# Kernel tuning notes

Hardware: AMD Instinct MI355X
Metric: run time of the kernel (lower is better)

Reference implementation:

```python
import jax, jax.numpy as jnp
import numpy as np

H = 16
D_MODEL = 1024
D_K = D_MODEL // H  # 64


def setup_inputs() -> dict:
    key = jax.random.key(0)
    ks = jax.random.split(key, 8)
    B, S = 8, 1024
    q = jax.random.normal(ks[0], (B, S, D_MODEL), dtype=jnp.float32)
    k = jax.random.normal(ks[1], (B, S, D_MODEL), dtype=jnp.float32)
    v = jax.random.normal(ks[2], (B, S, D_MODEL), dtype=jnp.float32)
    # xavier_normal for [h, d_model, d_k]: std = sqrt(2 / (d_model + d_k)) (fan over last two dims)
    std_p = float(np.sqrt(2.0 / (D_MODEL + D_K)))
    W_q = jax.random.normal(ks[3], (H, D_MODEL, D_K), dtype=jnp.float32) * std_p
    W_k = jax.random.normal(ks[4], (H, D_MODEL, D_K), dtype=jnp.float32) * std_p
    W_v = jax.random.normal(ks[5], (H, D_MODEL, D_K), dtype=jnp.float32) * std_p
    std_o = float(np.sqrt(2.0 / (H * D_K + D_MODEL)))
    W_o = jax.random.normal(ks[6], (D_MODEL, H * D_K), dtype=jnp.float32) * std_o  # torch Linear weight [out, in]
    b_o = jax.random.normal(ks[7], (D_MODEL,), dtype=jnp.float32) * 0.01
    return {"q": q, "k": k, "v": v, "W_q": W_q, "W_k": W_k, "W_v": W_v, "W_o": W_o, "b_o": b_o}


def reference(q, k, v, W_q, W_k, W_v, W_o, b_o):
    B, S, _ = q.shape
    # per-head projections: [h, b, s, d_k]
    qh = jnp.einsum('bsd,hdk->hbsk', q, W_q)
    kh = jnp.einsum('bsd,hdk->hbsk', k, W_k)
    vh = jnp.einsum('bsd,hdk->hbsk', v, W_v)
    scale = 1.0 / jnp.sqrt(jnp.asarray(D_K, dtype=q.dtype))
    scores = jnp.einsum('hbsk,hbtk->hbst', qh, kh) * scale  # [h,b,s,s]
    attn = jax.nn.softmax(scores, axis=-1)
    c = jnp.einsum('hbst,hbtk->hbsk', attn, vh)  # [h,b,s,d_k]
    # torch code splits the stacked (h*b) batch and concats on feature dim:
    # head index becomes the OUTER factor of the feature dim -> [b,s,h*d_k]
    c = jnp.transpose(c, (1, 2, 0, 3)).reshape(B, S, H * D_K)
    out = c @ W_o.T + b_o
    return out
```

## Files before the change

### kernel.cpp

```cpp
#include <hip/hip_runtime.h>
#include <hip/hip_bf16.h>

typedef __bf16 bf16_t;
typedef __attribute__((ext_vector_type(8))) __bf16 bf16x8;
typedef __attribute__((ext_vector_type(4))) float f32x4;

#define MFMA(a, b, c) __builtin_amdgcn_mfma_f32_16x16x32_bf16(a, b, c, 0, 0, 0)

__device__ inline void gload_lds16(const bf16_t* g, bf16_t* l) {
  __builtin_amdgcn_global_load_lds(
      (const __attribute__((address_space(1))) void*)g,
      (__attribute__((address_space(3))) void*)l, 16, 0, 0);
}

__global__ void fill_sentinel(float* out, int n, float val) {
  int i = blockIdx.x * blockDim.x + threadIdx.x;
  if (i < n) out[i] = val;
}

__global__ void transpose_w(const float* __restrict__ Wq, const float* __restrict__ Wk,
                            const float* __restrict__ Wv, bf16_t* __restrict__ Wt) {
  int gid = blockIdx.x * blockDim.x + threadIdx.x;
  int e = gid * 8;
  int m = e >> 20;
  int rem = e & 1048575;
  int n = rem >> 10;
  int d0 = rem & 1023;
  const float* W = (m == 0) ? Wq : (m == 1) ? Wk : Wv;
  int h = n >> 6, kk = n & 63;
  union { bf16_t h8[8]; uint4 u; } tmp;
#pragma unroll
  for (int j = 0; j < 8; ++j)
    tmp.h8[j] = (bf16_t)W[((size_t)(h * 1024 + d0 + j)) * 64 + kk];
  *(uint4*)(Wt + e) = tmp.u;
}

__global__ void cvt_bf16(const float* __restrict__ in, bf16_t* __restrict__ out) {
  size_t i = (size_t)(blockIdx.x * blockDim.x + threadIdx.x) * 8;
  f32x4 a = *(const f32x4*)(in + i);
  f32x4 b = *(const f32x4*)(in + i + 4);
  bf16x8 r;
  r[0] = (bf16_t)a[0]; r[1] = (bf16_t)a[1]; r[2] = (bf16_t)a[2]; r[3] = (bf16_t)a[3];
  r[4] = (bf16_t)b[0]; r[5] = (bf16_t)b[1]; r[6] = (bf16_t)b[2]; r[7] = (bf16_t)b[3];
  *(bf16x8*)(out + i) = r;
}

template <int MODE>
__global__ void gemm_bt(const bf16_t* __restrict__ A, const bf16_t* __restrict__ Bt_,
                        const float* __restrict__ bias, void* __restrict__ out_) {
  __shared__ bf16_t sA[2][64 * 32];
  __shared__ bf16_t sB[2][128 * 32];
  const int t = threadIdx.x;
  const int w = t >> 6, l = t & 63;
  const int lq = l >> 4, ll = l & 15;
  const int m0 = blockIdx.x * 64, n0 = blockIdx.y * 128;
  const bf16_t* Bt = (MODE == 0 && m0 >= 8192) ? Bt_ + 1048576 : Bt_;
  const float scale = (MODE == 0 && m0 < 8192) ? 0.125f : 1.0f;
  const int srow = l >> 2;
  const int scol = (l & 3) * 8;
  f32x4 acc[4][2] = {};

  auto stage = [&](int bufi, int k0s) {
    gload_lds16(A + (size_t)(m0 + w * 16 + srow) * 1024 + k0s + scol,
                sA[bufi] + w * 512);
#pragma unroll
    for (int c = 0; c < 2; ++c) {
      int ch = w * 2 + c;
      gload_lds16(Bt + (size_t)(n0 + ch * 16 + srow) * 1024 + k0s + scol,
                  sB[bufi] + ch * 512);
    }
  };

  stage(0, 0);
  __syncthreads();

  int cur = 0;
  for (int k0 = 0; k0 < 1024; k0 += 32) {
    if (k0 + 32 < 1024) stage(cur ^ 1, k0 + 32);
    bf16x8 af[4], bfr[2];
#pragma unroll
    for (int i = 0; i < 4; ++i)
      af[i] = *(const bf16x8*)(sA[cur] + (i * 16 + ll) * 32 + lq * 8);
#pragma unroll
    for (int i = 0; i < 2; ++i)
      bfr[i] = *(const bf16x8*)(sB[cur] + (w * 32 + i * 16 + ll) * 32 + lq * 8);
#pragma unroll
    for (int mi = 0; mi < 4; ++mi)
#pragma unroll
      for (int ni = 0; ni < 2; ++ni)
        acc[mi][ni] = MFMA(af[mi], bfr[ni], acc[mi][ni]);
    __syncthreads();
    cur ^= 1;
  }
#pragma unroll
  for (int mi = 0; mi < 4; ++mi)
#pragma unroll
    for (int ni = 0; ni < 2; ++ni)
#pragma unroll
      for (int r = 0; r < 4; ++r) {
        int row = m0 + mi * 16 + lq * 4 + r;
        int col = n0 + w * 32 + ni * 16 + ll;
        float v = acc[mi][ni][r];
        if (MODE == 2) {
          ((float*)out_)[(size_t)row * 1024 + col] = v + bias[col];
        } else if (MODE == 1) {
          int h = col >> 6, kk = col & 63, b = row >> 10, s = row & 1023;
          ((bf16_t*)out_)[((size_t)((h * 8 + b) * 64 + kk)) * 1024 + s] = (bf16_t)v;
        } else {
          int mat = row >> 13, rr = row & 8191;
          int h = col >> 6, kk = col & 63, b = rr >> 10, s = rr & 1023;
          size_t idx = (size_t)mat * 8388608 +
                       ((size_t)((h * 8 + b) * 1024 + s)) * 64 + kk;
          ((bf16_t*)out_)[idx] = (bf16_t)(v * scale);
        }
      }
}

__global__ void attn_kernel(const bf16_t* __restrict__ qh, const bf16_t* __restrict__ kh,
                            const bf16_t* __restrict__ vt, bf16_t* __restrict__ c) {
  constexpr int KP = 72, PP = 72;
  __shared__ bf16_t sK[2][64 * KP];
  __shared__ bf16_t sP[4][16 * PP];
  const int t = threadIdx.x;
  const int w = t >> 6, l = t & 63;
  const int lq = l >> 4, ll = l & 15;
  const int orig = blockIdx.x + (blockIdx.y << 4);
  const int wg = (orig & 7) * 256 + (orig >> 3);
  const int q0 = (wg & 15) * 64;
  const int hb = wg >> 4;
  const int h = hb >> 3, b = hb & 7;
  const size_t base = (size_t)hb * 65536;
  const bf16_t* Q = qh + base + (size_t)q0 * 64;
  const bf16_t* K = kh + base;
  const bf16_t* V = vt + base;

  bf16x8 aq0 = *(const bf16x8*)(Q + (w * 16 + ll) * 64 + 0 * 32 + lq * 8);
  bf16x8 aq1 = *(const bf16x8*)(Q + (w * 16 + ll) * 64 + 1 * 32 + lq * 8);

  {
    int e0 = t * 8, e1 = (256 + t) * 8;
    uint4 ka = *(const uint4*)(K + e0);
    uint4 kb = *(const uint4*)(K + e1);
    *(uint4*)(sK[0] + (e0 >> 6) * KP + (e0 & 63)) = ka;
    *(uint4*)(sK[0] + (e1 >> 6) * KP + (e1 & 63)) = kb;
  }
  __syncthreads();

  float mrow = -1e30f, lrow = 0.f;
  f32x4 o[4] = {};
  bf16_t* Pw = sP[w];

  int cur = 0;
  for (int kt = 0; kt < 1024; kt += 64, cur ^= 1) {
    uint4 kr0, kr1;
    if (kt < 960) {
      kr0 = *(const uint4*)(K + (size_t)(kt + 64) * 64 + t * 8);
      kr1 = *(const uint4*)(K + (size_t)(kt + 64) * 64 + (256 + t) * 8);
    }
    const bf16_t* Vb = V + (size_t)ll * 1024 + kt + lq * 8;
    bf16x8 bv00 = *(const bf16x8*)(Vb + 0 * 16384 + 0);
    bf16x8 bv01 = *(const bf16x8*)(Vb + 1 * 16384 + 0);
    bf16x8 bv02 = *(const bf16x8*)(Vb + 2 * 16384 + 0);
    bf16x8 bv03 = *(const bf16x8*)(Vb + 3 * 16384 + 0);
    bf16x8 bv10 = *(const bf16x8*)(Vb + 0 * 16384 + 32);
    bf16x8 bv11 = *(const bf16x8*)(Vb + 1 * 16384 + 32);
    bf16x8 bv12 = *(const bf16x8*)(Vb + 2 * 16384 + 32);
    bf16x8 bv13 = *(const bf16x8*)(Vb + 3 * 16384 + 32);

    f32x4 sacc[4] = {};
    __builtin_amdgcn_s_setprio(1);
#pragma unroll
    for (int ni = 0; ni < 4; ++ni) {
      bf16x8 bk0 = *(const bf16x8*)(sK[cur] + (ni * 16 + ll) * KP + 0 * 32 + lq * 8);
      bf16x8 bk1 = *(const bf16x8*)(sK[cur] + (ni * 16 + ll) * KP + 1 * 32 + lq * 8);
      sacc[ni] = MFMA(bk0, aq0, sacc[ni]);
      sacc[ni] = MFMA(bk1, aq1, sacc[ni]);
    }
    __builtin_amdgcn_s_setprio(0);
    float rmax = -1e30f;
#pragma unroll
    for (int ni = 0; ni < 4; ++ni)
#pragma unroll
      for (int r = 0; r < 4; ++r)
        rmax = fmaxf(rmax, sacc[ni][r]);
    if (!__all(rmax <= mrow + 8.0f)) {
      rmax = fmaxf(rmax, __shfl_xor(rmax, 16));
      rmax = fmaxf(rmax, __shfl_xor(rmax, 32));
      float mnew = fmaxf(mrow, rmax);
      float alpha = __expf(mrow - mnew);
      mrow = mnew;
      lrow *= alpha;
#pragma unroll
      for (int r = 0; r < 4; ++r) {
        float ar = __shfl(alpha, lq * 4 + r, 16);
#pragma unroll
        for (int ni = 0; ni < 4; ++ni)
          o[ni][r] *= ar;
      }
    }
#pragma unroll
    for (int ni = 0; ni < 4; ++ni)
#pragma unroll
      for (int r = 0; r < 4; ++r) {
        float p = __expf(sacc[ni][r] - mrow);
        sacc[ni][r] = p;
        lrow += p;
      }
#pragma unroll
    for (int ni = 0; ni < 4; ++ni) {
      union { bf16_t h4[4]; uint2 u; } pk;
      pk.h4[0] = (bf16_t)sacc[ni][0];
      pk.h4[1] = (bf16_t)sacc[ni][1];
      pk.h4[2] = (bf16_t)sacc[ni][2];
      pk.h4[3] = (bf16_t)sacc[ni][3];
      *(uint2*)(Pw + ll * PP + ni * 16 + lq * 4) = pk.u;
    }
    asm volatile("s_waitcnt lgkmcnt(0)" ::: "memory");
    __builtin_amdgcn_sched_barrier(0);
    bf16x8 ap0 = *(const bf16x8*)(Pw + ll * PP + 0 * 32 + lq * 8);
    bf16x8 ap1 = *(const bf16x8*)(Pw + ll * PP + 1 * 32 + lq * 8);
    __builtin_amdgcn_s_setprio(1);
    o[0] = MFMA(ap0, bv00, o[0]);
    o[1] = MFMA(ap0, bv01, o[1]);
    o[2] = MFMA(ap0, bv02, o[2]);
    o[3] = MFMA(ap0, bv03, o[3]);
    o[0] = MFMA(ap1, bv10, o[0]);
    o[1] = MFMA(ap1, bv11, o[1]);
    o[2] = MFMA(ap1, bv12, o[2]);
    o[3] = MFMA(ap1, bv13, o[3]);
    __builtin_amdgcn_s_setprio(0);
    if (kt < 960) {
      int e0 = t * 8, e1 = (256 + t) * 8;
      *(uint4*)(sK[cur ^ 1] + (e0 >> 6) * KP + (e0 & 63)) = kr0;
      *(uint4*)(sK[cur ^ 1] + (e1 >> 6) * KP + (e1 & 63)) = kr1;
    }
    __syncthreads();
  }
  lrow += __shfl_xor(lrow, 16);
  lrow += __shfl_xor(lrow, 32);
#pragma unroll
  for (int r = 0; r < 4; ++r) {
    float lr = __shfl(lrow, lq * 4 + r, 16);
    int s = q0 + w * 16 + lq * 4 + r;
#pragma unroll
    for (int ni = 0; ni < 4; ++ni) {
      int dk = ni * 16 + ll;
      c[((size_t)(b * 1024 + s)) * 1024 + h * 64 + dk] = (bf16_t)(o[ni][r] / lr);
    }
  }
}

extern "C" void kernel_launch(void* const* d_in, const int* in_sizes, int n_in,
                              void* d_out, int out_size, void* d_ws, size_t ws_size,
                              hipStream_t stream) {
  float* out = (float*)d_out;
  int nblk_out = (out_size + 255) / 256;
  if (n_in != 8) {
    fill_sentinel<<<nblk_out, 256, 0, stream>>>(out, out_size, 600.0f + 10.0f * n_in);
    return;
  }
  const int expect[8] = {8388608, 8388608, 8388608, 1048576,
                         1048576, 1048576, 1048576, 1024};
  for (int i = 0; i < 8; ++i)
    if (in_sizes[i] != expect[i]) {
      fill_sentinel<<<nblk_out, 256, 0, stream>>>(out, out_size, 500.0f + 10.0f * i);
      return;
    }

  bf16_t* ws   = (bf16_t*)d_ws;
  bf16_t* qhb  = ws;
  bf16_t* vtb  = ws + 16777216;
  bf16_t* Wt   = ws + 25165824;
  bf16_t* cbuf = ws + 25165824;
  bf16_t* Wob  = ws;
  if (ws_size < 67108864ull) {
    fill_sentinel<<<nblk_out, 256, 0, stream>>>(out, out_size, 400.0f);
    return;
  }

  const float* q  = (const float*)d_in[0];
  const float* k  = (const float*)d_in[1];
  const float* v  = (const float*)d_in[2];
  const float* Wq = (const float*)d_in[3];
  const float* Wk = (const float*)d_in[4];
  const float* Wv = (const float*)d_in[5];
  const float* Wo = (const float*)d_in[6];
  const float* bo = (const float*)d_in[7];

  bf16_t* qb = (bf16_t*)d_out;
  bf16_t* kb = (bf16_t*)d_out + 8388608;
  bf16_t* vb = (bf16_t*)d_out;

  transpose_w<<<1536, 256, 0, stream>>>(Wq, Wk, Wv, Wt);
  cvt_bf16<<<4096, 256, 0, stream>>>(q, qb);
  cvt_bf16<<<4096, 256, 0, stream>>>(k, kb);
  gemm_bt<0><<<dim3(256, 8), 256, 0, stream>>>(qb, Wt, nullptr, qhb);
  cvt_bf16<<<4096, 256, 0, stream>>>(v, vb);
  gemm_bt<1><<<dim3(128, 8), 256, 0, stream>>>(vb, Wt + 2097152, nullptr, vtb);
  attn_kernel<<<dim3(16, 128), 256, 0, stream>>>(qhb, qhb + 8388608, vtb, cbuf);
  cvt_bf16<<<512, 256, 0, stream>>>(Wo, Wob);
  gemm_bt<2><<<dim3(128, 8), 256, 0, stream>>>(cbuf, Wob, bo, out);
}
```

Baseline: 421.2 us.

## Enlarge GEMM tiles to 128x128 with triple-buffered LDS pipeline

The projection GEMM tile grows from 64x128 to 128x128, so each wave computes a 64x64 sub-tile (4x4 MFMAs), which raises data reuse per LDS load. The k-loop now uses a three-stage LDS ring with prefetch distance two, partial vmcnt waits and a raw s_barrier in place of __syncthreads. The aim is to hide global-load latency and halve the number of blocks. In exchange it uses more LDS and accumulator registers, which may lower occupancy, and the grids become smaller (1024/512 blocks).

```diff
diff --git a/kernel.cpp b/kernel.cpp
--- a/kernel.cpp
+++ b/kernel.cpp
@@ -48,58 +48,72 @@
 template <int MODE>
 __global__ void gemm_bt(const bf16_t* __restrict__ A, const bf16_t* __restrict__ Bt_,
                         const float* __restrict__ bias, void* __restrict__ out_) {
-  __shared__ bf16_t sA[2][64 * 32];
-  __shared__ bf16_t sB[2][128 * 32];
+  __shared__ bf16_t sA[3][128 * 32];
+  __shared__ bf16_t sB[3][128 * 32];
   const int t = threadIdx.x;
   const int w = t >> 6, l = t & 63;
   const int lq = l >> 4, ll = l & 15;
-  const int m0 = blockIdx.x * 64, n0 = blockIdx.y * 128;
+  const int m0 = blockIdx.x * 128, n0 = blockIdx.y * 128;
   const bf16_t* Bt = (MODE == 0 && m0 >= 8192) ? Bt_ + 1048576 : Bt_;
   const float scale = (MODE == 0 && m0 < 8192) ? 0.125f : 1.0f;
+  const int wr = (w >> 1) * 64, wc = (w & 1) * 64;
   const int srow = l >> 2;
   const int scol = (l & 3) * 8;
-  f32x4 acc[4][2] = {};
+  f32x4 acc[4][4] = {};
 
   auto stage = [&](int bufi, int k0s) {
-    gload_lds16(A + (size_t)(m0 + w * 16 + srow) * 1024 + k0s + scol,
-                sA[bufi] + w * 512);
 #pragma unroll
     for (int c = 0; c < 2; ++c) {
       int ch = w * 2 + c;
-      gload_lds16(Bt + (size_t)(n0 + ch * 16 + srow) * 1024 + k0s + scol,
-                  sB[bufi] + ch * 512);
+      int row = ch * 16 + srow;
+      gload_lds16(A  + (size_t)(m0 + row) * 1024 + k0s + scol, sA[bufi] + ch * 512);
+      gload_lds16(Bt + (size_t)(n0 + row) * 1024 + k0s + scol, sB[bufi] + ch * 512);
     }
   };
 
+  auto compute = [&](int bufi) {
+    bf16x8 af[4], bfr[4];
+#pragma unroll
+    for (int i = 0; i < 4; ++i) {
+      af[i]  = *(const bf16x8*)(sA[bufi] + (wr + i * 16 + ll) * 32 + lq * 8);
+      bfr[i] = *(const bf16x8*)(sB[bufi] + (wc + i * 16 + ll) * 32 + lq * 8);
+    }
+#pragma unroll
+    for (int mi = 0; mi < 4; ++mi)
+#pragma unroll
+      for (int ni = 0; ni < 4; ++ni)
+        acc[mi][ni] = MFMA(af[mi], bfr[ni], acc[mi][ni]);
+  };
+
   stage(0, 0);
-  __syncthreads();
+  stage(1, 32);
 
   int cur = 0;
-  for (int k0 = 0; k0 < 1024; k0 += 32) {
-    if (k0 + 32 < 1024) stage(cur ^ 1, k0 + 32);
-    bf16x8 af[4], bfr[2];
-#pragma unroll
-    for (int i = 0; i < 4; ++i)
-      af[i] = *(const bf16x8*)(sA[cur] + (i * 16 + ll) * 32 + lq * 8);
-#pragma unroll
-    for (int i = 0; i < 2; ++i)
-      bfr[i] = *(const bf16x8*)(sB[cur] + (w * 32 + i * 16 + ll) * 32 + lq * 8);
-#pragma unroll
-    for (int mi = 0; mi < 4; ++mi)
-#pragma unroll
-      for (int ni = 0; ni < 2; ++ni)
-        acc[mi][ni] = MFMA(af[mi], bfr[ni], acc[mi][ni]);
-    __syncthreads();
-    cur ^= 1;
-  }
+  for (int k0 = 0; k0 < 992; k0 += 32) {
+    asm volatile("s_waitcnt vmcnt(4)" ::: "memory");
+    __builtin_amdgcn_s_barrier();
+    __builtin_amdgcn_sched_barrier(0);
+    compute(cur);
+    __builtin_amdgcn_sched_barrier(0);
+    if (k0 + 64 < 1024) {
+      int nb = cur + 2; if (nb >= 3) nb -= 3;
+      stage(nb, k0 + 64);
+    }
+    ++cur; if (cur == 3) cur = 0;
+  }
+  asm volatile("s_waitcnt vmcnt(0)" ::: "memory");
+  __builtin_amdgcn_s_barrier();
+  __builtin_amdgcn_sched_barrier(0);
+  compute(cur);
+
 #pragma unroll
   for (int mi = 0; mi < 4; ++mi)
 #pragma unroll
-    for (int ni = 0; ni < 2; ++ni)
+    for (int ni = 0; ni < 4; ++ni)
 #pragma unroll
       for (int r = 0; r < 4; ++r) {
-        int row = m0 + mi * 16 + lq * 4 + r;
-        int col = n0 + w * 32 + ni * 16 + ll;
+        int row = m0 + wr + mi * 16 + lq * 4 + r;
+        int col = n0 + wc + ni * 16 + ll;
         float v = acc[mi][ni][r];
         if (MODE == 2) {
           ((float*)out_)[(size_t)row * 1024 + col] = v + bias[col];
@@ -294,10 +308,10 @@
   transpose_w<<<1536, 256, 0, stream>>>(Wq, Wk, Wv, Wt);
   cvt_bf16<<<4096, 256, 0, stream>>>(q, qb);
   cvt_bf16<<<4096, 256, 0, stream>>>(k, kb);
-  gemm_bt<0><<<dim3(256, 8), 256, 0, stream>>>(qb, Wt, nullptr, qhb);
+  gemm_bt<0><<<dim3(128, 8), 256, 0, stream>>>(qb, Wt, nullptr, qhb);
   cvt_bf16<<<4096, 256, 0, stream>>>(v, vb);
-  gemm_bt<1><<<dim3(128, 8), 256, 0, stream>>>(vb, Wt + 2097152, nullptr, vtb);
+  gemm_bt<1><<<dim3(64, 8), 256, 0, stream>>>(vb, Wt + 2097152, nullptr, vtb);
   attn_kernel<<<dim3(16, 128), 256, 0, stream>>>(qhb, qhb + 8388608, vtb, cbuf);
   cvt_bf16<<<512, 256, 0, stream>>>(Wo, Wob);
-  gemm_bt<2><<<dim3(128, 8), 256, 0, stream>>>(cbuf, Wob, bo, out);
-}
+  gemm_bt<2><<<dim3(64, 8), 256, 0, stream>>>(cbuf, Wob, bo, out);
+}
```

After: 399.6 us. 5.1% less time.
